# Kernel tuning notes

Hardware: AMD Instinct MI355X
Metric: run time of the kernel (lower is better)

## Reference

```python
import jax, jax.numpy as jnp
import numpy as np

N_NODES = 50000
N_EDGES = 800000
N_GRAPHS = 64
IN_DIM = 128
HID = 128
S, C = 4, 16
DIM1 = 3 * S * S  # 48
OUT_DIM = DIM1 * C  # 768


def gcn_conv(x, W, b, src, dst, w):
    """PyG GCNConv: linear transform, then sym-normalized aggregation with self-loops (weight 1)."""
    n = x.shape[0]
    h = x @ W  # [N, out]
    deg = jnp.zeros((n,), x.dtype).at[dst].add(w) + 1.0  # self-loop weight 1
    dinv = jax.lax.rsqrt(deg)
    norm = dinv[src] * w * dinv[dst]  # [E]
    agg = jnp.zeros_like(h).at[dst].add(h[src] * norm[:, None])
    agg = agg + h * (1.0 / deg)[:, None]  # self-loop messages
    return agg + b


def setup_inputs() -> dict:
    key = jax.random.key(0)
    ks = jax.random.split(key, 16)
    x = jax.random.normal(ks[0], (N_NODES, IN_DIM), jnp.float32)
    edge_index = jax.random.randint(ks[1], (2, N_EDGES), 0, N_NODES, jnp.int64)
    edge_attr = jax.random.uniform(ks[2], (N_EDGES,), jnp.float32)
    batch = jnp.sort(jax.random.randint(ks[3], (N_NODES,), 0, N_GRAPHS, jnp.int64))

    def glorot(k, fan_in, fan_out):
        s = np.sqrt(6.0 / (fan_in + fan_out)).astype(np.float32)
        return jax.random.uniform(k, (fan_in, fan_out), jnp.float32, -s, s)

    return {
        "x": x, "edge_index": edge_index, "edge_attr": edge_attr, "batch": batch,
        "W1": glorot(ks[4], IN_DIM, HID), "b1": jnp.zeros((HID,), jnp.float32),
        "W2": glorot(ks[5], HID, HID // 2), "b2": jnp.zeros((HID // 2,), jnp.float32),
        "W3": glorot(ks[6], HID // 2, HID // 4), "b3": jnp.zeros((HID // 4,), jnp.float32),
        "Wl": glorot(ks[7], HID // 4, OUT_DIM), "bl": jnp.zeros((OUT_DIM,), jnp.float32),
    }


def reference(x, edge_index, edge_attr, batch, W1, b1, W2, b2, W3, b3, Wl, bl):
    src, dst = edge_index[0], edge_index[1]
    w = edge_attr / edge_attr.max()
    h = jax.nn.relu(gcn_conv(x, W1, b1, src, dst, w))
    h = jax.nn.relu(gcn_conv(h, W2, b2, src, dst, w))
    h = jax.nn.relu(gcn_conv(h, W3, b3, src, dst, w))
    # global mean pool over graphs
    sums = jax.ops.segment_sum(h, batch, num_segments=N_GRAPHS)
    cnt = jax.ops.segment_sum(jnp.ones((h.shape[0],), h.dtype), batch, num_segments=N_GRAPHS)
    pooled = sums / jnp.maximum(cnt, 1.0)[:, None]
    out = pooled @ Wl + bl  # [G, OUT_DIM]
    return out.reshape(N_GRAPHS, DIM1, C)
```

## Files before the change

kernel.cpp:

```cpp
#include <hip/hip_runtime.h>
#include <hip/hip_bf16.h>

#define NN 50000
#define NE 800000
#define NG 64
#define OUTD 768

#define G1B ((NN + 63) / 64)
#define MAXB 128
#define SSEG 32
#define TTL 4
#define ESEG (NE / SSEG)
#define NTL (NN / TTL)
#define HRB (SSEG * TTL)

__device__ __forceinline__ float bflo(unsigned int u) { return __uint_as_float(u << 16); }
__device__ __forceinline__ float bfhi(unsigned int u) { return __uint_as_float(u & 0xffff0000u); }
__device__ __forceinline__ unsigned short f2bf(float f) {
    unsigned int u = __float_as_uint(f);
    return (unsigned short)((u + 0x7fffu + ((u >> 16) & 1u)) >> 16);
}
__device__ __forceinline__ unsigned int pack2bf(float lo, float hi) {
    return (unsigned int)f2bf(lo) | ((unsigned int)f2bf(hi) << 16);
}

typedef __attribute__((ext_vector_type(8))) short bf16x8;
typedef __attribute__((ext_vector_type(4))) float f32x4;
union FragU { uint4 u4; bf16x8 v; };

template <int K, int N>
constexpr int mfma_lds_bytes() { return (K / 32) * (N / 16) * 1024; }

template <int K, int N, typename TX>
__device__ __forceinline__ void mfma_gemm_body(char* smem,
                                               const TX* __restrict__ X,
                                               const float* __restrict__ W,
                                               unsigned short* __restrict__ Y,
                                               int nRows, int bx) {
    constexpr int NCT = N / 16;
    constexpr int KS = K / 32;
    const int tid = threadIdx.x;

    for (int q = tid; q < KS * NCT * 64; q += 256) {
        int lane = q & 63;
        int fi = q >> 6;
        int ct = fi % NCT, kc = fi / NCT;
        int col = ct * 16 + (lane & 15);
        int kb = kc * 32 + ((lane >> 4) << 3);
        uint4 w;
        w.x = pack2bf(W[(size_t)(kb + 0) * N + col], W[(size_t)(kb + 1) * N + col]);
        w.y = pack2bf(W[(size_t)(kb + 2) * N + col], W[(size_t)(kb + 3) * N + col]);
        w.z = pack2bf(W[(size_t)(kb + 4) * N + col], W[(size_t)(kb + 5) * N + col]);
        w.w = pack2bf(W[(size_t)(kb + 6) * N + col], W[(size_t)(kb + 7) * N + col]);
        *(uint4*)(smem + (size_t)q * 16) = w;
    }
    __syncthreads();

    const int lane = tid & 63;
    const int wv = tid >> 6;
    const int m = lane & 15;
    const int quad = lane >> 4;
    const int row = bx * 64 + wv * 16 + m;
    const bool rowok = row < nRows;
    const TX* xr = X + (size_t)(rowok ? row : 0) * K;

    f32x4 acc[NCT];
#pragma unroll
    for (int ct = 0; ct < NCT; ++ct) acc[ct] = (f32x4){0.f, 0.f, 0.f, 0.f};

#pragma unroll
    for (int kc = 0; kc < KS; ++kc) {
        const int k0 = kc * 32 + quad * 8;
        FragU a;
        if constexpr (sizeof(TX) == 4) {
            float4 a0 = make_float4(0.f, 0.f, 0.f, 0.f), a1 = a0;
            if (rowok) {
                a0 = *(const float4*)(xr + k0);
                a1 = *(const float4*)(xr + k0 + 4);
            }
            a.u4 = make_uint4(pack2bf(a0.x, a0.y), pack2bf(a0.z, a0.w),
                              pack2bf(a1.x, a1.y), pack2bf(a1.z, a1.w));
        } else {
            a.u4 = rowok ? *(const uint4*)(xr + k0) : make_uint4(0, 0, 0, 0);
        }
#pragma unroll
        for (int ct = 0; ct < NCT; ++ct) {
            FragU b;
            b.u4 = *(const uint4*)(smem + ((size_t)(kc * NCT + ct) * 64 + lane) * 16);
            acc[ct] = __builtin_amdgcn_mfma_f32_16x16x32_bf16(a.v, b.v, acc[ct], 0, 0, 0);
        }
    }

    const int orowb = bx * 64 + wv * 16 + quad * 4;
#pragma unroll
    for (int ct = 0; ct < NCT; ++ct) {
        int col = ct * 16 + m;
#pragma unroll
        for (int r = 0; r < 4; ++r) {
            int orow = orowb + r;
            if (orow < nRows) Y[(size_t)orow * N + col] = f2bf(acc[ct][r]);
        }
    }
}

template <int K, int N, typename TX>
__global__ __launch_bounds__(256) void mfma_gemm_kernel(const TX* __restrict__ X,
                                                        const float* __restrict__ W,
                                                        unsigned short* __restrict__ Y,
                                                        int nRows) {
    extern __shared__ char smem[];
    mfma_gemm_body<K, N>(smem, X, W, Y, nRows, blockIdx.x);
}

__global__ __launch_bounds__(256) void fused1_kernel(const float* __restrict__ x,
                                                     const float* __restrict__ W1,
                                                     unsigned short* __restrict__ bufA,
                                                     const float* __restrict__ ea,
                                                     unsigned int* wmax,
                                                     const int* __restrict__ dst,
                                                     int* __restrict__ rank,
                                                     unsigned short* __restrict__ pcnt) {
    extern __shared__ char smem[];
    const int b = blockIdx.x;
    if (b < G1B) {
        mfma_gemm_body<128, 128>(smem, x, W1, bufA, NN, b);
    } else if (b < G1B + MAXB) {
        float* red = (float*)smem;
        const int bb = b - G1B;
        const float4* ea4 = (const float4*)ea;
        float m = 0.0f;
        for (int i = bb * 256 + threadIdx.x; i < NE / 4; i += MAXB * 256) {
            float4 v = ea4[i];
            m = fmaxf(fmaxf(m, fmaxf(v.x, v.y)), fmaxf(v.z, v.w));
        }
        red[threadIdx.x] = m;
        __syncthreads();
        for (int off = 128; off > 0; off >>= 1) {
            if (threadIdx.x < off)
                red[threadIdx.x] = fmaxf(red[threadIdx.x], red[threadIdx.x + off]);
            __syncthreads();
        }
        if (threadIdx.x == 0) atomicMax(wmax, __float_as_uint(red[0]));
    } else {
        const int b2 = b - G1B - MAXB;
        const int seg = b2 >> 2;
        const int tile = b2 & 3;
        unsigned int* lcnt = (unsigned int*)smem;
        for (int i = threadIdx.x; i < NTL / 2; i += 256) lcnt[i] = 0;
        __syncthreads();
        const int base = seg * ESEG;
        const int nlo = tile * NTL;
        const int4* dst4 = (const int4*)(dst + base);
        for (int g = threadIdx.x; g < ESEG / 4; g += 256) {
            const int4 v = dst4[g];
            const int e0 = base + g * 4;
            const int dd[4] = {v.x, v.y, v.z, v.w};
#pragma unroll
            for (int j = 0; j < 4; ++j) {
                int d = dd[j] - nlo;
                if ((unsigned)d < (unsigned)NTL) {
                    unsigned sh = (unsigned)(d & 1) << 4;
                    unsigned old = atomicAdd(&lcnt[d >> 1], 1u << sh);
                    rank[e0 + j] = (int)((old >> sh) & 0xffffu);
                }
            }
        }
        __syncthreads();
        unsigned int* prow32 = (unsigned int*)(pcnt + (size_t)seg * NN + nlo);
        for (int i = threadIdx.x; i < NTL / 2; i += 256) prow32[i] = lcnt[i];
    }
}

__global__ __launch_bounds__(256) void comb_kernel(unsigned short* __restrict__ pcnt,
                                                   int* __restrict__ hist,
                                                   int* __restrict__ blocksum) {
    __shared__ int red[256];
    int n = blockIdx.x * 256 + threadIdx.x;
    int run = 0;
    if (n < NN) {
#pragma unroll
        for (int s = 0; s < SSEG; ++s) {
            size_t idx = (size_t)s * NN + n;
            int v = pcnt[idx];
            pcnt[idx] = (unsigned short)run;
            run += v;
        }
        hist[n] = run;
    }
    red[threadIdx.x] = (n < NN) ? run : 0;
    __syncthreads();
    for (int off = 128; off > 0; off >>= 1) {
        if (threadIdx.x < off) red[threadIdx.x] += red[threadIdx.x + off];
        __syncthreads();
    }
    if (threadIdx.x == 0) blocksum[blockIdx.x] = red[0];
}

__global__ __launch_bounds__(256) void scan3_kernel(const int* __restrict__ hist,
                                                    const int* __restrict__ blocksum,
                                                    int* __restrict__ rowptr, int n, int nb) {
    __shared__ int sb[256];
    __shared__ int s[256];
    const int tid = threadIdx.x;
    int bv = (tid < nb) ? blocksum[tid] : 0;
    sb[tid] = bv;
    __syncthreads();
    for (int off = 1; off < 256; off <<= 1) {
        int t = (tid >= off) ? sb[tid - off] : 0;
        __syncthreads();
        sb[tid] += t;
        __syncthreads();
    }
    const int boff = (blockIdx.x > 0) ? sb[blockIdx.x - 1] : 0;
    const int total = sb[nb - 1];

    int i = blockIdx.x * 256 + tid;
    int v = (i < n) ? hist[i] : 0;
    s[tid] = v;
    __syncthreads();
    for (int off = 1; off < 256; off <<= 1) {
        int t = (tid >= off) ? s[tid - off] : 0;
        __syncthreads();
        s[tid] += t;
        __syncthreads();
    }
    if (i < n) rowptr[i] = boff + s[tid] - v;
    if (blockIdx.x == 0 && tid == 0) rowptr[n] = total;
}

__global__ void scat_kernel(const int* __restrict__ src, const int* __restrict__ dst,
                            const float* __restrict__ ea,
                            const int* __restrict__ rowptr,
                            const unsigned short* __restrict__ pcnt,
                            const int* __restrict__ rank,
                            int2* __restrict__ epack, int nE4) {
    int g = blockIdx.x * blockDim.x + threadIdx.x;
    if (g >= nE4) return;
    const int s = (g * 4) / ESEG;
    const size_t pb = (size_t)s * NN;
    const int4 d4 = ((const int4*)dst)[g];
    const int4 s4 = ((const int4*)src)[g];
    const float4 e4 = ((const float4*)ea)[g];
    const int4 r4 = ((const int4*)rank)[g];
    const int dd[4] = {d4.x, d4.y, d4.z, d4.w};
    const int ss[4] = {s4.x, s4.y, s4.z, s4.w};
    const float ee[4] = {e4.x, e4.y, e4.z, e4.w};
    const int rr[4] = {r4.x, r4.y, r4.z, r4.w};
#pragma unroll
    for (int j = 0; j < 4; ++j) {
        int pos = rowptr[dd[j]] + (int)pcnt[pb + dd[j]] + rr[j];
        epack[pos] = make_int2(ss[j], __float_as_int(ee[j]));
    }
}

__global__ void deg_kernel(const int2* __restrict__ epack, const int* __restrict__ rowptr,
                           const unsigned int* __restrict__ wmax,
                           float* __restrict__ nrm, float* __restrict__ invdeg, int n) {
    int i = blockIdx.x * blockDim.x + threadIdx.x;
    if (i >= n) return;
    float rw = 1.0f / __uint_as_float(*wmax);
    float srw = sqrtf(rw);
    int s0 = rowptr[i], s1 = rowptr[i + 1];
    float sa = 0.f, sb = 0.f;
    int e = s0;
    for (; e + 2 <= s1; e += 2) {
        sa += __int_as_float(epack[e].y);
        sb += __int_as_float(epack[e + 1].y);
    }
    if (e < s1) sa += __int_as_float(epack[e].y);
    float d = fmaf(sa + sb, rw, 1.0f);
    nrm[i] = rsqrtf(d) * srw;
    invdeg[i] = 1.0f / d;
}

template <int D, bool PRE>
__global__ __launch_bounds__(256) void agg_kernel(const unsigned short* __restrict__ H,
                                                  const int* __restrict__ rowptr,
                                                  int2* __restrict__ epack,
                                                  const float* __restrict__ invdeg,
                                                  const float* __restrict__ nrm,
                                                  const float* __restrict__ bias,
                                                  unsigned short* __restrict__ out,
                                                  int nNodes) {
    constexpr int LPE = D / 8;
    constexpr int EPW = 64 / LPE;
    const int lane = threadIdx.x & 63;
    const int n = (blockIdx.x << 2) | (threadIdx.x >> 6);
    if (n >= nNodes) return;
    const int esub = lane / LPE;
    const int f8 = (lane % LPE) * 8;
    const int s0 = rowptr[n];
    const int cnt = rowptr[n + 1] - s0;
    int2* ep = epack + s0;
    const float dn = PRE ? 1.0f : nrm[n];

    float a[8] = {};
#define AGG8(c_, u_)                                                            \
    a[0] = fmaf(c_, bflo(u_.x), a[0]); a[1] = fmaf(c_, bfhi(u_.x), a[1]);       \
    a[2] = fmaf(c_, bflo(u_.y), a[2]); a[3] = fmaf(c_, bfhi(u_.y), a[3]);       \
    a[4] = fmaf(c_, bflo(u_.z), a[4]); a[5] = fmaf(c_, bfhi(u_.z), a[5]);       \
    a[6] = fmaf(c_, bflo(u_.w), a[6]); a[7] = fmaf(c_, bfhi(u_.w), a[7]);

    int kb = 0;
    for (; kb + 4 * EPW <= cnt; kb += 4 * EPW) {
        const int2 p0 = ep[kb + 0 * EPW + esub];
        const int2 p1 = ep[kb + 1 * EPW + esub];
        const int2 p2 = ep[kb + 2 * EPW + esub];
        const int2 p3 = ep[kb + 3 * EPW + esub];
        const uint4 u0 = *(const uint4*)(H + (size_t)p0.x * D + f8);
        const uint4 u1 = *(const uint4*)(H + (size_t)p1.x * D + f8);
        const uint4 u2 = *(const uint4*)(H + (size_t)p2.x * D + f8);
        const uint4 u3 = *(const uint4*)(H + (size_t)p3.x * D + f8);
        float c0, c1, c2, c3;
        if constexpr (PRE) {
            c0 = __int_as_float(p0.y); c1 = __int_as_float(p1.y);
            c2 = __int_as_float(p2.y); c3 = __int_as_float(p3.y);
        } else {
            c0 = nrm[p0.x] * __int_as_float(p0.y) * dn;
            c1 = nrm[p1.x] * __int_as_float(p1.y) * dn;
            c2 = nrm[p2.x] * __int_as_float(p2.y) * dn;
            c3 = nrm[p3.x] * __int_as_float(p3.y) * dn;
            if (f8 == 0) {
                ep[kb + 0 * EPW + esub].y = __float_as_int(c0);
                ep[kb + 1 * EPW + esub].y = __float_as_int(c1);
                ep[kb + 2 * EPW + esub].y = __float_as_int(c2);
                ep[kb + 3 * EPW + esub].y = __float_as_int(c3);
            }
        }
        AGG8(c0, u0) AGG8(c1, u1) AGG8(c2, u2) AGG8(c3, u3)
    }
    for (; kb + 2 * EPW <= cnt; kb += 2 * EPW) {
        const int2 p0 = ep[kb + esub];
        const int2 p1 = ep[kb + EPW + esub];
        const uint4 u0 = *(const uint4*)(H + (size_t)p0.x * D + f8);
        const uint4 u1 = *(const uint4*)(H + (size_t)p1.x * D + f8);
        float c0, c1;
        if constexpr (PRE) {
            c0 = __int_as_float(p0.y); c1 = __int_as_float(p1.y);
        } else {
            c0 = nrm[p0.x] * __int_as_float(p0.y) * dn;
            c1 = nrm[p1.x] * __int_as_float(p1.y) * dn;
            if (f8 == 0) {
                ep[kb + esub].y = __float_as_int(c0);
                ep[kb + EPW + esub].y = __float_as_int(c1);
            }
        }
        AGG8(c0, u0) AGG8(c1, u1)
    }
    for (; kb < cnt; kb += EPW) {
        const int idx = kb + esub;
        const bool ok = idx < cnt;
        const int2 p = ok ? ep[idx] : make_int2(n, 0);
        const uint4 u = *(const uint4*)(H + (size_t)p.x * D + f8);
        float c;
        if constexpr (PRE) {
            c = ok ? __int_as_float(p.y) : 0.f;
        } else {
            c = ok ? nrm[p.x] * __int_as_float(p.y) * dn : 0.f;
            if (ok && f8 == 0) ep[idx].y = __float_as_int(c);
        }
        AGG8(c, u)
    }
#undef AGG8
#pragma unroll
    for (int off = LPE; off < 64; off <<= 1) {
#pragma unroll
        for (int j = 0; j < 8; ++j) a[j] += __shfl_xor(a[j], off);
    }
    if (esub == 0) {
        const float id = invdeg[n];
        const uint4 un = *(const uint4*)(H + (size_t)n * D + f8);
        const float4 b0 = *(const float4*)(bias + f8);
        const float4 b1 = *(const float4*)(bias + f8 + 4);
        float o[8];
        o[0] = fmaxf(fmaf(id, bflo(un.x), a[0]) + b0.x, 0.f);
        o[1] = fmaxf(fmaf(id, bfhi(un.x), a[1]) + b0.y, 0.f);
        o[2] = fmaxf(fmaf(id, bflo(un.y), a[2]) + b0.z, 0.f);
        o[3] = fmaxf(fmaf(id, bfhi(un.y), a[3]) + b0.w, 0.f);
        o[4] = fmaxf(fmaf(id, bflo(un.z), a[4]) + b1.x, 0.f);
        o[5] = fmaxf(fmaf(id, bfhi(un.z), a[5]) + b1.y, 0.f);
        o[6] = fmaxf(fmaf(id, bflo(un.w), a[6]) + b1.z, 0.f);
        o[7] = fmaxf(fmaf(id, bfhi(un.w), a[7]) + b1.w, 0.f);
        uint4 w;
        w.x = pack2bf(o[0], o[1]);
        w.y = pack2bf(o[2], o[3]);
        w.z = pack2bf(o[4], o[5]);
        w.w = pack2bf(o[6], o[7]);
        *(uint4*)(out + (size_t)n * D + f8) = w;
    }
}

__global__ __launch_bounds__(1024) void poolfin_kernel(const unsigned short* __restrict__ h,
                                                       const int* __restrict__ batch,
                                                       const float* __restrict__ Wl,
                                                       const float* __restrict__ bl,
                                                       float* __restrict__ out, int n) {
    const int g = blockIdx.x;
    int lo = 0, hi = n;
    while (lo < hi) { int m = (lo + hi) >> 1; if (batch[m] < g) lo = m + 1; else hi = m; }
    const int start = lo;
    lo = start; hi = n;
    while (lo < hi) { int m = (lo + hi) >> 1; if (batch[m] < g + 1) lo = m + 1; else hi = m; }
    const int end = lo;

    __shared__ float part[1024];
    __shared__ float spool[32];
    const int f = threadIdx.x & 31;
    const int r = threadIdx.x >> 5;
    float acc = 0.f;
    for (int i = start + r; i < end; i += 32)
        acc += __uint_as_float((unsigned int)h[(size_t)i * 32 + f] << 16);
    part[threadIdx.x] = acc;
    __syncthreads();
    if (threadIdx.x < 32) {
        float s = 0.f;
#pragma unroll
        for (int q = 0; q < 32; ++q) s += part[q * 32 + f];
        float inv = 1.0f / fmaxf((float)(end - start), 1.0f);
        spool[f] = s * inv;
    }
    __syncthreads();
    if (threadIdx.x < OUTD) {
        const int o = threadIdx.x;
        float a2 = bl[o];
#pragma unroll
        for (int k = 0; k < 32; ++k)
            a2 = fmaf(spool[k], Wl[k * OUTD + o], a2);
        out[(size_t)g * OUTD + o] = a2;
    }
}

extern "C" void kernel_launch(void* const* d_in, const int* in_sizes, int n_in,
                              void* d_out, int out_size, void* d_ws, size_t ws_size,
                              hipStream_t stream) {
    const float* x = (const float*)d_in[0];
    const int* eidx = (const int*)d_in[1];
    const float* ea = (const float*)d_in[2];
    const int* batch = (const int*)d_in[3];
    const float* W1 = (const float*)d_in[4];
    const float* b1 = (const float*)d_in[5];
    const float* W2 = (const float*)d_in[6];
    const float* b2 = (const float*)d_in[7];
    const float* W3 = (const float*)d_in[8];
    const float* b3 = (const float*)d_in[9];
    const float* Wl = (const float*)d_in[10];
    const float* bl = (const float*)d_in[11];
    const int* src = eidx;
    const int* dst = eidx + NE;

    char* p = (char*)d_ws;
    auto take = [&](size_t bytes) {
        char* r = p;
        p += (bytes + 255) & ~(size_t)255;
        return r;
    };
    float* nrm = (float*)take(NN * 4);
    float* invdeg = (float*)take(NN * 4);
    int* hist = (int*)take(NN * 4);
    int* rowptr = (int*)take((NN + 1) * 4);
    int* blocksum = (int*)take(256 * 4);
    int2* epack = (int2*)take((size_t)NE * 8);
    unsigned int* wmax = (unsigned int*)take(4);
    unsigned short* bufA = (unsigned short*)take((size_t)NN * 128 * 2);
    unsigned short* bufB = (unsigned short*)take((size_t)NN * 128 * 2);
    int* rank = (int*)bufB;
    unsigned short* pcnt = (unsigned short*)((char*)bufB + (size_t)NE * 4 + 256);

    const int nblk = (NN + 255) / 256;
    const int e4blk = (NE / 4 + 255) / 256;

    hipMemsetAsync(wmax, 0, 4, stream);

    constexpr int LDS1 = mfma_lds_bytes<128, 128>();
    static_assert(LDS1 >= NTL * 2, "HR branch LDS (packed u16 counters) must fit");
    fused1_kernel<<<G1B + MAXB + HRB, 256, LDS1, stream>>>(x, W1, bufA, ea, wmax,
                                                           dst, rank, pcnt);
    comb_kernel<<<nblk, 256, 0, stream>>>(pcnt, hist, blocksum);
    scan3_kernel<<<nblk, 256, 0, stream>>>(hist, blocksum, rowptr, NN, nblk);
    scat_kernel<<<e4blk, 256, 0, stream>>>(src, dst, ea, rowptr, pcnt, rank, epack, NE / 4);
    deg_kernel<<<nblk, 256, 0, stream>>>(epack, rowptr, wmax, nrm, invdeg, NN);

    agg_kernel<128, false><<<(NN + 3) / 4, 256, 0, stream>>>(bufA, rowptr, epack, invdeg, nrm, b1, bufB, NN);
    mfma_gemm_kernel<128, 64, unsigned short>
        <<<G1B, 256, mfma_lds_bytes<128, 64>(), stream>>>(bufB, W2, bufA, NN);
    agg_kernel<64, true><<<(NN + 3) / 4, 256, 0, stream>>>(bufA, rowptr, epack, invdeg, nrm, b2, bufB, NN);
    mfma_gemm_kernel<64, 32, unsigned short>
        <<<G1B, 256, mfma_lds_bytes<64, 32>(), stream>>>(bufB, W3, bufA, NN);
    agg_kernel<32, true><<<(NN + 3) / 4, 256, 0, stream>>>(bufA, rowptr, epack, invdeg, nrm, b3, bufB, NN);

    poolfin_kernel<<<NG, 1024, 0, stream>>>(bufB, batch, Wl, bl, (float*)d_out, NN);
}
```

Baseline: 261.7 us.

## Fold source-side norm into layer outputs and drop per-edge coefficient write-back

The symmetric normalization is refactored so each layer's output is pre-scaled by the node's dinv. The next layer's aggregation then only needs the raw edge weight, with no per-edge nrm gather and no write-back of coefficients into epack during layer 1. A self-loop coefficient array (selfc) is computed in deg_kernel, and the destination-side norm is applied once per node in the epilogue. This removes scattered edge writes and gathers, but rescales intermediate bf16 activations, which may slightly change rounding.

Result: faster. 255.0 us (-2.6%).

```diff
diff --git a/kernel.cpp b/kernel.cpp
--- a/kernel.cpp
+++ b/kernel.cpp
@@ -255,7 +255,8 @@
 
 __global__ void deg_kernel(const int2* __restrict__ epack, const int* __restrict__ rowptr,
                            const unsigned int* __restrict__ wmax,
-                           float* __restrict__ nrm, float* __restrict__ invdeg, int n) {
+                           float* __restrict__ nrm, float* __restrict__ invdeg,
+                           float* __restrict__ selfc, int n) {
     int i = blockIdx.x * blockDim.x + threadIdx.x;
     if (i >= n) return;
     float rw = 1.0f / __uint_as_float(*wmax);
@@ -269,16 +270,19 @@
     }
     if (e < s1) sa += __int_as_float(epack[e].y);
     float d = fmaf(sa + sb, rw, 1.0f);
-    nrm[i] = rsqrtf(d) * srw;
+    float rs = rsqrtf(d);
+    nrm[i] = rs * srw;
     invdeg[i] = 1.0f / d;
-}
-
-template <int D, bool PRE>
+    selfc[i] = rs / srw;
+}
+
+template <int D, int MODE>
 __global__ __launch_bounds__(256) void agg_kernel(const unsigned short* __restrict__ H,
                                                   const int* __restrict__ rowptr,
-                                                  int2* __restrict__ epack,
+                                                  const int2* __restrict__ epack,
+                                                  const float* __restrict__ nrm,
                                                   const float* __restrict__ invdeg,
-                                                  const float* __restrict__ nrm,
+                                                  const float* __restrict__ selfc,
                                                   const float* __restrict__ bias,
                                                   unsigned short* __restrict__ out,
                                                   int nNodes) {
@@ -291,8 +295,7 @@
     const int f8 = (lane % LPE) * 8;
     const int s0 = rowptr[n];
     const int cnt = rowptr[n + 1] - s0;
-    int2* ep = epack + s0;
-    const float dn = PRE ? 1.0f : nrm[n];
+    const int2* ep = epack + s0;
 
     float a[8] = {};
 #define AGG8(c_, u_)                                                            \
@@ -300,6 +303,7 @@
     a[2] = fmaf(c_, bflo(u_.y), a[2]); a[3] = fmaf(c_, bfhi(u_.y), a[3]);       \
     a[4] = fmaf(c_, bflo(u_.z), a[4]); a[5] = fmaf(c_, bfhi(u_.z), a[5]);       \
     a[6] = fmaf(c_, bflo(u_.w), a[6]); a[7] = fmaf(c_, bfhi(u_.w), a[7]);
+#define COEF(p_) (MODE == 0 ? nrm[p_.x] * __int_as_float(p_.y) : __int_as_float(p_.y))
 
     int kb = 0;
     for (; kb + 4 * EPW <= cnt; kb += 4 * EPW) {
@@ -311,22 +315,10 @@
         const uint4 u1 = *(const uint4*)(H + (size_t)p1.x * D + f8);
         const uint4 u2 = *(const uint4*)(H + (size_t)p2.x * D + f8);
         const uint4 u3 = *(const uint4*)(H + (size_t)p3.x * D + f8);
-        float c0, c1, c2, c3;
-        if constexpr (PRE) {
-            c0 = __int_as_float(p0.y); c1 = __int_as_float(p1.y);
-            c2 = __int_as_float(p2.y); c3 = __int_as_float(p3.y);
-        } else {
-            c0 = nrm[p0.x] * __int_as_float(p0.y) * dn;
-            c1 = nrm[p1.x] * __int_as_float(p1.y) * dn;
-            c2 = nrm[p2.x] * __int_as_float(p2.y) * dn;
-            c3 = nrm[p3.x] * __int_as_float(p3.y) * dn;
-            if (f8 == 0) {
-                ep[kb + 0 * EPW + esub].y = __float_as_int(c0);
-                ep[kb + 1 * EPW + esub].y = __float_as_int(c1);
-                ep[kb + 2 * EPW + esub].y = __float_as_int(c2);
-                ep[kb + 3 * EPW + esub].y = __float_as_int(c3);
-            }
-        }
+        const float c0 = COEF(p0);
+        const float c1 = COEF(p1);
+        const float c2 = COEF(p2);
+        const float c3 = COEF(p3);
         AGG8(c0, u0) AGG8(c1, u1) AGG8(c2, u2) AGG8(c3, u3)
     }
     for (; kb + 2 * EPW <= cnt; kb += 2 * EPW) {
@@ -334,17 +326,8 @@
         const int2 p1 = ep[kb + EPW + esub];
         const uint4 u0 = *(const uint4*)(H + (size_t)p0.x * D + f8);
         const uint4 u1 = *(const uint4*)(H + (size_t)p1.x * D + f8);
-        float c0, c1;
-        if constexpr (PRE) {
-            c0 = __int_as_float(p0.y); c1 = __int_as_float(p1.y);
-        } else {
-            c0 = nrm[p0.x] * __int_as_float(p0.y) * dn;
-            c1 = nrm[p1.x] * __int_as_float(p1.y) * dn;
-            if (f8 == 0) {
-                ep[kb + esub].y = __float_as_int(c0);
-                ep[kb + EPW + esub].y = __float_as_int(c1);
-            }
-        }
+        const float c0 = COEF(p0);
+        const float c1 = COEF(p1);
         AGG8(c0, u0) AGG8(c1, u1)
     }
     for (; kb < cnt; kb += EPW) {
@@ -352,15 +335,10 @@
         const bool ok = idx < cnt;
         const int2 p = ok ? ep[idx] : make_int2(n, 0);
         const uint4 u = *(const uint4*)(H + (size_t)p.x * D + f8);
-        float c;
-        if constexpr (PRE) {
-            c = ok ? __int_as_float(p.y) : 0.f;
-        } else {
-            c = ok ? nrm[p.x] * __int_as_float(p.y) * dn : 0.f;
-            if (ok && f8 == 0) ep[idx].y = __float_as_int(c);
-        }
+        const float c = ok ? COEF(p) : 0.f;
         AGG8(c, u)
     }
+#undef COEF
 #undef AGG8
 #pragma unroll
     for (int off = LPE; off < 64; off <<= 1) {
@@ -368,19 +346,24 @@
         for (int j = 0; j < 8; ++j) a[j] += __shfl_xor(a[j], off);
     }
     if (esub == 0) {
-        const float id = invdeg[n];
+        const float dn = nrm[n];
+        const float sc = (MODE == 0) ? invdeg[n] : selfc[n];
         const uint4 un = *(const uint4*)(H + (size_t)n * D + f8);
         const float4 b0 = *(const float4*)(bias + f8);
         const float4 b1 = *(const float4*)(bias + f8 + 4);
         float o[8];
-        o[0] = fmaxf(fmaf(id, bflo(un.x), a[0]) + b0.x, 0.f);
-        o[1] = fmaxf(fmaf(id, bfhi(un.x), a[1]) + b0.y, 0.f);
-        o[2] = fmaxf(fmaf(id, bflo(un.y), a[2]) + b0.z, 0.f);
-        o[3] = fmaxf(fmaf(id, bfhi(un.y), a[3]) + b0.w, 0.f);
-        o[4] = fmaxf(fmaf(id, bflo(un.z), a[4]) + b1.x, 0.f);
-        o[5] = fmaxf(fmaf(id, bfhi(un.z), a[5]) + b1.y, 0.f);
-        o[6] = fmaxf(fmaf(id, bflo(un.w), a[6]) + b1.z, 0.f);
-        o[7] = fmaxf(fmaf(id, bfhi(un.w), a[7]) + b1.w, 0.f);
+        o[0] = fmaxf(fmaf(dn, a[0], fmaf(sc, bflo(un.x), b0.x)), 0.f);
+        o[1] = fmaxf(fmaf(dn, a[1], fmaf(sc, bfhi(un.x), b0.y)), 0.f);
+        o[2] = fmaxf(fmaf(dn, a[2], fmaf(sc, bflo(un.y), b0.z)), 0.f);
+        o[3] = fmaxf(fmaf(dn, a[3], fmaf(sc, bfhi(un.y), b0.w)), 0.f);
+        o[4] = fmaxf(fmaf(dn, a[4], fmaf(sc, bflo(un.z), b1.x)), 0.f);
+        o[5] = fmaxf(fmaf(dn, a[5], fmaf(sc, bfhi(un.z), b1.y)), 0.f);
+        o[6] = fmaxf(fmaf(dn, a[6], fmaf(sc, bflo(un.w), b1.z)), 0.f);
+        o[7] = fmaxf(fmaf(dn, a[7], fmaf(sc, bfhi(un.w), b1.w)), 0.f);
+        if constexpr (MODE != 2) {
+#pragma unroll
+            for (int j = 0; j < 8; ++j) o[j] *= dn;
+        }
         uint4 w;
         w.x = pack2bf(o[0], o[1]);
         w.y = pack2bf(o[2], o[3]);
@@ -456,6 +439,7 @@
     };
     float* nrm = (float*)take(NN * 4);
     float* invdeg = (float*)take(NN * 4);
+    float* selfc = (float*)take(NN * 4);
     int* hist = (int*)take(NN * 4);
     int* rowptr = (int*)take((NN + 1) * 4);
     int* blocksum = (int*)take(256 * 4);
@@ -478,15 +462,18 @@
     comb_kernel<<<nblk, 256, 0, stream>>>(pcnt, hist, blocksum);
     scan3_kernel<<<nblk, 256, 0, stream>>>(hist, blocksum, rowptr, NN, nblk);
     scat_kernel<<<e4blk, 256, 0, stream>>>(src, dst, ea, rowptr, pcnt, rank, epack, NE / 4);
-    deg_kernel<<<nblk, 256, 0, stream>>>(epack, rowptr, wmax, nrm, invdeg, NN);
-
-    agg_kernel<128, false><<<(NN + 3) / 4, 256, 0, stream>>>(bufA, rowptr, epack, invdeg, nrm, b1, bufB, NN);
+    deg_kernel<<<nblk, 256, 0, stream>>>(epack, rowptr, wmax, nrm, invdeg, selfc, NN);
+
+    agg_kernel<128, 0><<<(NN + 3) / 4, 256, 0, stream>>>(bufA, rowptr, epack, nrm,
+                                                         invdeg, selfc, b1, bufB, NN);
     mfma_gemm_kernel<128, 64, unsigned short>
         <<<G1B, 256, mfma_lds_bytes<128, 64>(), stream>>>(bufB, W2, bufA, NN);
-    agg_kernel<64, true><<<(NN + 3) / 4, 256, 0, stream>>>(bufA, rowptr, epack, invdeg, nrm, b2, bufB, NN);
+    agg_kernel<64, 1><<<(NN + 3) / 4, 256, 0, stream>>>(bufA, rowptr, epack, nrm,
+                                                        invdeg, selfc, b2, bufB, NN);
     mfma_gemm_kernel<64, 32, unsigned short>
         <<<G1B, 256, mfma_lds_bytes<64, 32>(), stream>>>(bufB, W3, bufA, NN);
-    agg_kernel<32, true><<<(NN + 3) / 4, 256, 0, stream>>>(bufA, rowptr, epack, invdeg, nrm, b3, bufB, NN);
+    agg_kernel<32, 2><<<(NN + 3) / 4, 256, 0, stream>>>(bufA, rowptr, epack, nrm,
+                                                        invdeg, selfc, b3, bufB, NN);
 
     poolfin_kernel<<<NG, 1024, 0, stream>>>(bufB, batch, Wl, bl, (float*)d_out, NN);
 }
```
